# Optimization experiments

Measured on AMD Instinct MI355X. Metric: run time of the kernel, lower is better.

The kernel has to match this reference:

```python
import jax, jax.numpy as jnp
import numpy as np
from jax import lax

EXP = 3          # exp_size
TOPK = 9         # top_number
DS = 4           # down_sample (stride & kernel of conv_down)
UP = 4           # up_sample
C_CH = 64        # c
BN_EPS = 1e-5


def conv2d(x, w, b, stride, pad):
    y = lax.conv_general_dilated(x, w, (stride, stride), ((pad, pad), (pad, pad)),
                                 dimension_numbers=('NCHW', 'OIHW', 'NCHW'))
    return y + b[None, :, None, None]


def bnorm(x, g, b, m, v):
    scale = g / jnp.sqrt(v + BN_EPS)
    return (x - m[None, :, None, None]) * scale[None, :, None, None] + b[None, :, None, None]


def get_feat(x1, H, W):
    # x1: [B, C, L] flattened downsampled features
    B, C, L = x1.shape
    win = 2 * EXP + 1
    xt = jnp.transpose(x1, (0, 2, 1))                      # [B, L, C]
    # euclidean distance -> similarity 1/(1+d)
    sq = jnp.sum(xt * xt, axis=-1)                         # [B, L]
    d2 = sq[:, :, None] + sq[:, None, :] - 2.0 * jnp.einsum('blc,bmc->blm', xt, xt)
    dist = jnp.sqrt(jnp.maximum(d2, 1e-12))
    sim = 1.0 / (1.0 + dist)                               # [B, L, L]
    pad = jnp.pad(sim.reshape(B, L, H, W),
                  ((0, 0), (0, 0), (EXP, EXP), (EXP, EXP)),
                  constant_values=1e20)                    # [B, L, H+2e, W+2e]
    l = jnp.arange(L)
    row, col = l // W, l % W
    d = jnp.arange(win)
    off_i = jnp.repeat(d, win)
    off_j = jnp.tile(d, win)
    ii = row[:, None] + off_i[None, :]                     # [L, P] padded coords
    jj = col[:, None] + off_j[None, :]
    win_val = pad[:, l[:, None], ii, jj]                   # [B, L, P]
    # topk SMALLEST similarity (most dissimilar); padded 1e20 never selected
    _, idx = lax.top_k(-win_val, TOPK)                     # [B, L, k]
    h_bias = idx // win - EXP
    w_bias = idx % win - EXP
    Hf = row[None, :, None] + h_bias
    Wf = col[None, :, None] + w_bias
    index = Hf * W + Wf                                    # [B, L, k] in [0, L)
    b_idx = jnp.arange(B)[:, None, None]
    x_final = xt[b_idx, index]                             # [B, L, k, C]
    return x_final


def setup_inputs() -> dict:
    key = jax.random.key(0)
    ks = jax.random.split(key, 6)
    c = C_CH
    f32 = jnp.float32
    x = jax.random.normal(ks[0], (4, c, 256, 256), f32)
    wd = jax.random.normal(ks[1], (c, c, DS, DS), f32) * 0.05
    bd = jnp.zeros((c,), f32)
    w1 = jax.random.normal(ks[2], (c, 2 * c, 3, 3), f32) * 0.05
    b1 = jnp.zeros((c,), f32)
    wa = jax.random.normal(ks[3], (c, c, 1, 1), f32) * 0.05
    ones, zeros = jnp.ones((c,), f32), jnp.zeros((c,), f32)
    return dict(x=x,
                wd=wd, bd=bd, bnd_g=ones, bnd_b=zeros, bnd_m=zeros, bnd_v=ones,
                w1=w1, b1=b1, bn1_g=ones, bn1_b=zeros, bn1_m=zeros, bn1_v=ones,
                wa=wa, bna_g=ones, bna_b=zeros, bna_m=zeros, bna_v=ones)


def reference(x, wd, bd, bnd_g, bnd_b, bnd_m, bnd_v,
              w1, b1, bn1_g, bn1_b, bn1_m, bn1_v,
              wa, bna_g, bna_b, bna_m, bna_v):
    # conv_down: Conv(k=DS, s=DS, p=0) + BN + ReLU
    x1 = jax.nn.relu(bnorm(conv2d(x, wd, bd, DS, 0), bnd_g, bnd_b, bnd_m, bnd_v))
    B, C, H, W = x1.shape
    L = H * W
    xf = x1.reshape(B, C, L)
    x_final = get_feat(xf, H, W)                           # [B, L, k, C]
    xt = jnp.transpose(xf, (0, 2, 1))                      # [B, L, C]
    out = jnp.mean(x_final - xt[:, :, None, :], axis=2)    # [B, L, C]
    out_img = jnp.transpose(out, (0, 2, 1)).reshape(B, C, H, W)
    cat = jnp.concatenate([x1, out_img], axis=1)           # [B, 2C, H, W]
    # SENet: conv3x3 + BN + ReLU, global-avg-pool attention
    feat = jax.nn.relu(bnorm(conv2d(cat, w1, b1, 1, 1), bn1_g, bn1_b, bn1_m, bn1_v))
    att = jnp.mean(feat, axis=(2, 3), keepdims=True)       # [B, C, 1, 1]
    att = lax.conv_general_dilated(att, wa, (1, 1), ((0, 0), (0, 0)),
                                   dimension_numbers=('NCHW', 'OIHW', 'NCHW'))
    att = jax.nn.sigmoid(bnorm(att, bna_g, bna_b, bna_m, bna_v))
    out = feat * att
    # F.interpolate bilinear, align_corners=False == half-pixel resize
    return jax.image.resize(out, (B, C, H * UP, W * UP), method='bilinear')
```

## Files before the change

kernel.cpp:

```cpp
#include <hip/hip_runtime.h>
#include <hip/hip_bf16.h>
#include <stdint.h>

__device__ __forceinline__ float* catp(float* o, int p) {
    return o + (size_t)(p & 255) * 65536 + 4096 + ((p >> 8) << 12);
}
__device__ __forceinline__ double* x1hp(float* o, int q) {
    return (double*)(o + (size_t)q * 65536 + 16384);
}
__device__ __forceinline__ float wtv(const float* o, int kk, int co) {
    return o[(size_t)(kk >> 3) * 65536 + 25600 + (kk & 7) * 64 + co];
}
__device__ __forceinline__ double* wd64p(float* o, int k) {
    return (double*)(o + (size_t)(k >> 2) * 65536 + 26624) + (k & 3) * 64;
}

__global__ __launch_bounds__(256) void k0_wtrans(const float* __restrict__ w1, const float* __restrict__ wd,
                                                 float* __restrict__ o) {
    int idx = blockIdx.x * 256 + threadIdx.x;
    if (idx < 73728) {
        int co = idx & 63, kk = idx >> 6;
        o[(size_t)(kk >> 3) * 65536 + 25600 + (kk & 7) * 64 + co] = w1[co * 1152 + kk];
    } else if (idx < 139264) {
        int j = idx - 73728;
        int co = j & 63, k = j >> 6;
        wd64p(o, k)[co] = (double)wd[co * 1024 + k];
    }
}

__global__ __launch_bounds__(256) void k1_convds(
    const float* __restrict__ x, const float* __restrict__ bd,
    const float* __restrict__ g, const float* __restrict__ be,
    const float* __restrict__ m, const float* __restrict__ v,
    float* __restrict__ o)
{
    __shared__ __align__(16) double wlds[2][32 * 64];
    __shared__ __align__(16) double xlds[2][32 * 32];
    int blk = blockIdx.x;
    int jh = blk & 1, i = (blk >> 1) & 63, b = blk >> 7;
    int t = threadIdx.x;
    int tj = t & 15, tc = t >> 4;
    int s_f4j = t & 31, s_ky = (t >> 5) & 3, s_ciL = t >> 7;
    int s_kq = (s_ciL * 16 + s_ky * 4) * 32 + s_f4j;

    double acc[4][2];
    #pragma unroll
    for (int c = 0; c < 4; ++c) { acc[c][0] = 0.0; acc[c][1] = 0.0; }

    double wreg[8];
    float4 xreg;
    #pragma unroll
    for (int u = 0; u < 8; ++u) {
        int idx = t + u * 256;
        wreg[u] = wd64p(o, (idx >> 6))[idx & 63];
    }
    xreg = *(const float4*)(x + (((size_t)(b * 64 + s_ciL) * 256 + (i * 4 + s_ky)) * 256 + jh * 128 + s_f4j * 4));
    #pragma unroll
    for (int u = 0; u < 8; ++u) {
        int idx = t + u * 256;
        wlds[0][(idx >> 6) * 64 + (idx & 63)] = wreg[u];
    }
    xlds[0][s_kq]      = (double)xreg.x;
    xlds[0][s_kq + 32] = (double)xreg.y;
    xlds[0][s_kq + 64] = (double)xreg.z;
    xlds[0][s_kq + 96] = (double)xreg.w;
    __syncthreads();

    for (int p = 0; p < 32; ++p) {
        int cur = p & 1;
        if (p + 1 < 32) {
            #pragma unroll
            for (int u = 0; u < 8; ++u) {
                int idx = t + u * 256;
                wreg[u] = wd64p(o, (p + 1) * 32 + (idx >> 6))[idx & 63];
            }
            xreg = *(const float4*)(x + (((size_t)(b * 64 + (p + 1) * 2 + s_ciL) * 256 + (i * 4 + s_ky)) * 256 + jh * 128 + s_f4j * 4));
        }
        const double* wb = wlds[cur];
        const double* xb = xlds[cur];
        #pragma unroll
        for (int ciL = 0; ciL < 2; ++ciL) {
            #pragma unroll
            for (int ky = 0; ky < 4; ++ky) {
                int kq = ciL * 16 + ky * 4;
                double w_[4][4], x_[4][2];
                #pragma unroll
                for (int kx = 0; kx < 4; ++kx) {
                    const double* wp = wb + (kq + kx) * 64;
                    const double* xp = xb + (kq + kx) * 32;
                    double2 wa0 = *(const double2*)(wp + tc * 2);
                    double2 wa1 = *(const double2*)(wp + tc * 2 + 32);
                    double2 xa0 = *(const double2*)(xp + tj * 2);
                    w_[kx][0] = wa0.x; w_[kx][1] = wa0.y; w_[kx][2] = wa1.x; w_[kx][3] = wa1.y;
                    x_[kx][0] = xa0.x; x_[kx][1] = xa0.y;
                }
                #pragma unroll
                for (int c = 0; c < 4; ++c)
                    #pragma unroll
                    for (int jj = 0; jj < 2; ++jj)
                        acc[c][jj] = fma(w_[0][c], x_[0][jj],
                                     fma(w_[1][c], x_[1][jj],
                                     fma(w_[2][c], x_[2][jj],
                                     fma(w_[3][c], x_[3][jj], acc[c][jj]))));
            }
        }
        if (p + 1 < 32) {
            int nxt = (p + 1) & 1;
            #pragma unroll
            for (int u = 0; u < 8; ++u) {
                int idx = t + u * 256;
                wlds[nxt][(idx >> 6) * 64 + (idx & 63)] = wreg[u];
            }
            xlds[nxt][s_kq]      = (double)xreg.x;
            xlds[nxt][s_kq + 32] = (double)xreg.y;
            xlds[nxt][s_kq + 64] = (double)xreg.z;
            xlds[nxt][s_kq + 96] = (double)xreg.w;
            __syncthreads();
        }
    }
    #pragma unroll
    for (int c = 0; c < 4; ++c) {
        int co = ((c >> 1) << 5) + tc * 2 + (c & 1);
        double sc = (double)g[co] / sqrt((double)v[co] + 1e-5);
        double sh = (double)bd[co] - (double)m[co];
        double bb = (double)be[co];
        double o0v = fmax(0.0, (acc[c][0] + sh) * sc + bb);
        double o1v = fmax(0.0, (acc[c][1] + sh) * sc + bb);
        int pos0 = i * 64 + jh * 32 + tj * 2;
        float* cp = catp(o, b * 128 + co);
        *(float2*)(cp + pos0) = make_float2((float)o0v, (float)o1v);
        double* xh = x1hp(o, b * 64 + co);
        *(double2*)(xh + pos0) = make_double2(o0v, o1v);
    }
}

__global__ __launch_bounds__(512) void k2_feat(float* __restrict__ o)
{
    __shared__ __align__(16) char smem[29568];
    __shared__ double sqd[7 * 64];
    __shared__ int sels[64 * 9];
    double* tile_d = (double*)smem;
    double* d2s = (double*)smem;
    float* tileq = (float*)smem;
    int blk = blockIdx.x;
    int b = blk >> 6, i = blk & 63;
    int t = threadIdx.x;
    int lane = t & 63, wv = t >> 6;

    double dacc[7];
    #pragma unroll
    for (int k = 0; k < 7; ++k) dacc[k] = 0.0;
    double sq_own = 0.0;

    for (int q = 0; q < 8; ++q) {
        __syncthreads();
        for (int s = t; s < 1792; s += 512) {
            int rc = s >> 5, c2 = s & 31;
            int r = rc >> 3, c = rc & 7;
            int gr = i - 3 + r;
            if (gr >= 0 && gr <= 63) {
                const double* src = x1hp(o, b * 64 + q * 8 + c);
                *(double2*)(tile_d + rc * 66 + c2 * 2) = *(const double2*)(src + gr * 64 + c2 * 2);
            }
        }
        __syncthreads();
        if (t < 448) {
            int r = t >> 6, col = t & 63;
            int gr = i - 3 + r;
            if (gr >= 0 && gr <= 63) {
                double s = 0.0;
                #pragma unroll
                for (int c = 0; c < 8; ++c) {
                    double xv = tile_d[(r * 8 + c) * 66 + col];
                    s = fma(xv, xv, s);
                }
                sq_own += s;
            }
        }
        double xlq[8];
        #pragma unroll
        for (int c = 0; c < 8; ++c) xlq[c] = tile_d[(24 + c) * 66 + lane];
        #pragma unroll
        for (int k = 0; k < 7; ++k) {
            int oo = wv + 8 * k;
            if (oo < 49) {
                int oi = oo / 7 - 3, oj = oo % 7 - 3;
                int mi = i + oi, mj = lane + oj;
                if (mi >= 0 && mi <= 63 && mj >= 0 && mj <= 63) {
                    int r = oi + 3;
                    double dot = 0.0;
                    #pragma unroll
                    for (int c = 0; c < 8; ++c) dot = fma(xlq[c], tile_d[(r * 8 + c) * 66 + mj], dot);
                    dacc[k] += dot;
                }
            }
        }
    }
    __syncthreads();
    if (t < 448) sqd[t] = sq_own;
    __syncthreads();
    #pragma unroll
    for (int k = 0; k < 7; ++k) {
        int oo = wv + 8 * k;
        if (oo < 49) {
            int oi = oo / 7 - 3, oj = oo % 7 - 3;
            int mi = i + oi, mj = lane + oj;
            double d2 = -1e300;
            if (mi >= 0 && mi <= 63 && mj >= 0 && mj <= 63)
                d2 = sqd[192 + lane] + sqd[(oi + 3) * 64 + mj] - 2.0 * dacc[k];
            d2s[lane * 50 + oo] = d2;
        }
    }
    __syncthreads();
    if (wv == 0) {
        unsigned long long mask = 0ull;
        for (int k = 0; k < 9; ++k) {
            double best = -1e308; int bi = 0;
            for (int oo = 0; oo < 49; ++oo) {
                if ((mask >> oo) & 1ull) continue;
                double vv = d2s[lane * 50 + oo];
                if (vv > best) { best = vv; bi = oo; }
            }
            mask |= (1ull << bi);
            sels[lane * 9 + k] = bi;
        }
    }
    __syncthreads();
    int rk[9], cj[9];
    #pragma unroll
    for (int k = 0; k < 9; ++k) {
        int oo = sels[lane * 9 + k];
        rk[k] = oo / 7;
        cj[k] = lane + (oo % 7) - 3;
    }
    for (int q = 0; q < 8; ++q) {
        __syncthreads();
        for (int s = t; s < 896; s += 512) {
            int rc = s >> 4, x4 = s & 15;
            int r = rc >> 3, c = rc & 7;
            int gr = i - 3 + r;
            if (gr >= 0 && gr <= 63)
                *(float4*)(tileq + rc * 68 + x4 * 4) =
                    *(const float4*)(catp(o, b * 128 + q * 8 + c) + gr * 64 + x4 * 4);
        }
        __syncthreads();
        {
            int c = wv;
            float s = 0.f;
            #pragma unroll
            for (int k = 0; k < 9; ++k) s += tileq[(rk[k] * 8 + c) * 68 + cj[k]];
            float outv = s * (1.f / 9.f) - tileq[(24 + c) * 68 + lane];
            catp(o, b * 128 + 64 + q * 8 + c)[i * 64 + lane] = outv;
        }
    }
}

__global__ __launch_bounds__(512) void k3_conv(
    float* __restrict__ o, const float* __restrict__ b1,
    const float* __restrict__ g, const float* __restrict__ be,
    const float* __restrict__ m, const float* __restrict__ v)
{
    __shared__ __align__(16) float wlds[8 * 9 * 64];
    __shared__ __align__(16) float xlds[3 * 8 * 40];
    int blk = blockIdx.x;
    int jh = blk & 1, i = (blk >> 1) & 63, b = blk >> 7;
    int t = threadIdx.x;
    int co = t & 63, jg = t >> 6;
    float acc0 = 0.f, acc1 = 0.f, acc2 = 0.f, acc3 = 0.f;
    const float4 z4 = make_float4(0.f, 0.f, 0.f, 0.f);
    for (int st = 0; st < 16; ++st) {
        __syncthreads();
        for (int idx = t; idx < 4608; idx += 512) {
            int kk = st * 72 + (idx >> 6);
            wlds[idx] = wtv(o, kk, idx & 63);
        }
        for (int f = t; f < 240; f += 512) {
            int x4 = f % 10, rc = f / 10;
            int ry = rc >> 3, cl = rc & 7;
            int gr = i - 1 + ry;
            int col0 = jh * 32 - 4 + x4 * 4;
            float4 val = z4;
            if (gr >= 0 && gr <= 63 && col0 >= 0 && col0 <= 60)
                val = *(const float4*)(catp(o, b * 128 + st * 8 + cl) + gr * 64 + col0);
            *(float4*)(xlds + rc * 40 + x4 * 4) = val;
        }
        __syncthreads();
        for (int cl = 0; cl < 8; ++cl) {
            #pragma unroll
            for (int ry = 0; ry < 3; ++ry) {
                float w0  = wlds[(cl * 9 + ry * 3 + 0) * 64 + co];
                float w1f = wlds[(cl * 9 + ry * 3 + 1) * 64 + co];
                float w2  = wlds[(cl * 9 + ry * 3 + 2) * 64 + co];
                const float* xr = xlds + (ry * 8 + cl) * 40 + jg * 4;
                float4 q0 = *(const float4*)(xr);
                float4 q1 = *(const float4*)(xr + 4);
                float4 q2 = *(const float4*)(xr + 8);
                float xv[12] = { q0.x,q0.y,q0.z,q0.w, q1.x,q1.y,q1.z,q1.w, q2.x,q2.y,q2.z,q2.w };
                acc0 = fmaf(w0, xv[3], fmaf(w1f, xv[4], fmaf(w2, xv[5], acc0)));
                acc1 = fmaf(w0, xv[4], fmaf(w1f, xv[5], fmaf(w2, xv[6], acc1)));
                acc2 = fmaf(w0, xv[5], fmaf(w1f, xv[6], fmaf(w2, xv[7], acc2)));
                acc3 = fmaf(w0, xv[6], fmaf(w1f, xv[7], fmaf(w2, xv[8], acc3)));
            }
        }
    }
    float sc = g[co] * rsqrtf(v[co] + 1e-5f);
    float sh = b1[co] - m[co];
    float bb = be[co];
    float4 ov;
    ov.x = fmaxf(0.f, fmaf(acc0 + sh, sc, bb));
    ov.y = fmaxf(0.f, fmaf(acc1 + sh, sc, bb));
    ov.z = fmaxf(0.f, fmaf(acc2 + sh, sc, bb));
    ov.w = fmaxf(0.f, fmaf(acc3 + sh, sc, bb));
    *(float4*)(o + (size_t)(b * 64 + co) * 65536 + i * 64 + jh * 32 + jg * 4) = ov;
}

__global__ __launch_bounds__(256) void k4_mean(float* __restrict__ o) {
    int q = blockIdx.x, t = threadIdx.x;
    const float* p = o + (size_t)q * 65536;
    float s = 0.f;
    for (int k = t; k < 4096; k += 256) s += p[k];
    #pragma unroll
    for (int off = 32; off > 0; off >>= 1) s += __shfl_down(s, off, 64);
    __shared__ float red[4];
    if ((t & 63) == 0) red[t >> 6] = s;
    __syncthreads();
    if (t == 0) o[(size_t)q * 65536 + 12288] = (red[0] + red[1] + red[2] + red[3]) * (1.f / 4096.f);
}

__global__ __launch_bounds__(256) void k4_att(float* __restrict__ o, const float* __restrict__ wa,
    const float* __restrict__ g, const float* __restrict__ be, const float* __restrict__ m, const float* __restrict__ v) {
    int t = threadIdx.x;
    int b = t >> 6, co = t & 63;
    const float* wr = wa + co * 64;
    float s = 0.f;
    for (int ci = 0; ci < 64; ++ci) s = fmaf(wr[ci], o[(size_t)(b * 64 + ci) * 65536 + 12288], s);
    float sc = g[co] * rsqrtf(v[co] + 1e-5f);
    float y = fmaf(s - m[co], sc, be[co]);
    o[(size_t)t * 65536 + 12289] = 1.f / (1.f + expf(-y));
}

__global__ __launch_bounds__(1024) void k5_up(float* __restrict__ o) {
    __shared__ __align__(16) float fplane[4096];
    int bc = blockIdx.x;
    int t = threadIdx.x;
    float* slot = o + (size_t)bc * 65536;
    *(float4*)(fplane + t * 4) = *(const float4*)(slot + t * 4);
    float att = slot[12289];
    __syncthreads();
    int ox = t & 255, oyc = t >> 8;
    float fx = ox * 0.25f - 0.375f;
    int ix = (int)floorf(fx);
    float wx = fx - (float)ix;
    int x0 = ix < 0 ? 0 : ix;
    int x1 = (ix + 1 > 63) ? 63 : ix + 1;
    for (int oy = oyc * 64; oy < oyc * 64 + 64; ++oy) {
        float fy = oy * 0.25f - 0.375f;
        int iy = (int)floorf(fy);
        float wy = fy - (float)iy;
        int y0 = iy < 0 ? 0 : iy;
        int y1 = (iy + 1 > 63) ? 63 : iy + 1;
        float a  = fplane[y0 * 64 + x0], b_ = fplane[y0 * 64 + x1];
        float c_ = fplane[y1 * 64 + x0], d_ = fplane[y1 * 64 + x1];
        float top = a + wx * (b_ - a);
        float bot = c_ + wx * (d_ - c_);
        float val = (top + wy * (bot - top)) * att;
        slot[oy * 256 + ox] = val;
    }
}

extern "C" void kernel_launch(void* const* d_in, const int* in_sizes, int n_in,
                              void* d_out, int out_size, void* d_ws, size_t ws_size,
                              hipStream_t stream) {
    const float* x     = (const float*)d_in[0];
    const float* wd    = (const float*)d_in[1];
    const float* bd    = (const float*)d_in[2];
    const float* bnd_g = (const float*)d_in[3];
    const float* bnd_b = (const float*)d_in[4];
    const float* bnd_m = (const float*)d_in[5];
    const float* bnd_v = (const float*)d_in[6];
    const float* w1    = (const float*)d_in[7];
    const float* b1    = (const float*)d_in[8];
    const float* bn1_g = (const float*)d_in[9];
    const float* bn1_b = (const float*)d_in[10];
    const float* bn1_m = (const float*)d_in[11];
    const float* bn1_v = (const float*)d_in[12];
    const float* wa    = (const float*)d_in[13];
    const float* bna_g = (const float*)d_in[14];
    const float* bna_b = (const float*)d_in[15];
    const float* bna_m = (const float*)d_in[16];
    const float* bna_v = (const float*)d_in[17];

    float* o = (float*)d_out;

    hipLaunchKernelGGL(k0_wtrans, dim3(544), dim3(256), 0, stream, w1, wd, o);
    hipLaunchKernelGGL(k1_convds, dim3(512), dim3(256), 0, stream,
                       x, bd, bnd_g, bnd_b, bnd_m, bnd_v, o);
    hipLaunchKernelGGL(k2_feat, dim3(256), dim3(512), 0, stream, o);
    hipLaunchKernelGGL(k3_conv, dim3(512), dim3(512), 0, stream,
                       o, b1, bn1_g, bn1_b, bn1_m, bn1_v);
    hipLaunchKernelGGL(k4_mean, dim3(256), dim3(256), 0, stream, o);
    hipLaunchKernelGGL(k4_att, dim3(1), dim3(256), 0, stream,
                       o, wa, bna_g, bna_b, bna_m, bna_v);
    hipLaunchKernelGGL(k5_up, dim3(256), dim3(1024), 0, stream, o);
}
```

Before: 241.5 us.

## Double-buffer weight and input tiles in 3x3 conv kernel via register prefetch

The conv3x3 kernel now keeps two LDS buffers for weights and input rows. While the current channel slice is being computed, it loads the next slice into registers and stores it to the other buffer afterwards, leaving one barrier per stage instead of two. This is meant to hide global load latency behind the FMA loop. It costs double the LDS and extra registers (9 floats plus a float4), which may lower occupancy.

```diff
diff --git a/kernel.cpp b/kernel.cpp
--- a/kernel.cpp
+++ b/kernel.cpp
@@ -260,38 +260,57 @@
     const float* __restrict__ g, const float* __restrict__ be,
     const float* __restrict__ m, const float* __restrict__ v)
 {
-    __shared__ __align__(16) float wlds[8 * 9 * 64];
-    __shared__ __align__(16) float xlds[3 * 8 * 40];
+    __shared__ __align__(16) float wlds[2][8 * 9 * 64];
+    __shared__ __align__(16) float xlds[2][3 * 8 * 40];
     int blk = blockIdx.x;
     int jh = blk & 1, i = (blk >> 1) & 63, b = blk >> 7;
     int t = threadIdx.x;
     int co = t & 63, jg = t >> 6;
     float acc0 = 0.f, acc1 = 0.f, acc2 = 0.f, acc3 = 0.f;
     const float4 z4 = make_float4(0.f, 0.f, 0.f, 0.f);
+    bool xact = t < 240;
+    int x_x4 = t % 10, x_rc = t / 10;
+    int x_ry = x_rc >> 3;
+    int x_cl = x_rc & 7;
+    int x_gr = i - 1 + x_ry;
+    int x_col0 = jh * 32 - 4 + x_x4 * 4;
+    bool x_ok = xact && x_gr >= 0 && x_gr <= 63 && x_col0 >= 0 && x_col0 <= 60;
+
+    float wreg[9];
+    float4 xreg = z4;
+    #pragma unroll
+    for (int u = 0; u < 9; ++u) {
+        int idx = t + u * 512;
+        wreg[u] = wtv(o, (idx >> 6), idx & 63);
+    }
+    if (x_ok) xreg = *(const float4*)(catp(o, b * 128 + x_cl) + x_gr * 64 + x_col0);
+    #pragma unroll
+    for (int u = 0; u < 9; ++u) {
+        int idx = t + u * 512;
+        wlds[0][idx] = wreg[u];
+    }
+    if (xact) *(float4*)(&xlds[0][x_rc * 40 + x_x4 * 4]) = x_ok ? xreg : z4;
+    __syncthreads();
+
     for (int st = 0; st < 16; ++st) {
-        __syncthreads();
-        for (int idx = t; idx < 4608; idx += 512) {
-            int kk = st * 72 + (idx >> 6);
-            wlds[idx] = wtv(o, kk, idx & 63);
-        }
-        for (int f = t; f < 240; f += 512) {
-            int x4 = f % 10, rc = f / 10;
-            int ry = rc >> 3, cl = rc & 7;
-            int gr = i - 1 + ry;
-            int col0 = jh * 32 - 4 + x4 * 4;
-            float4 val = z4;
-            if (gr >= 0 && gr <= 63 && col0 >= 0 && col0 <= 60)
-                val = *(const float4*)(catp(o, b * 128 + st * 8 + cl) + gr * 64 + col0);
-            *(float4*)(xlds + rc * 40 + x4 * 4) = val;
-        }
-        __syncthreads();
+        int cur = st & 1;
+        if (st + 1 < 16) {
+            #pragma unroll
+            for (int u = 0; u < 9; ++u) {
+                int idx = t + u * 512;
+                wreg[u] = wtv(o, (st + 1) * 72 + (idx >> 6), idx & 63);
+            }
+            if (x_ok) xreg = *(const float4*)(catp(o, b * 128 + (st + 1) * 8 + x_cl) + x_gr * 64 + x_col0);
+        }
+        const float* wb = wlds[cur];
+        const float* xb = xlds[cur];
         for (int cl = 0; cl < 8; ++cl) {
             #pragma unroll
             for (int ry = 0; ry < 3; ++ry) {
-                float w0  = wlds[(cl * 9 + ry * 3 + 0) * 64 + co];
-                float w1f = wlds[(cl * 9 + ry * 3 + 1) * 64 + co];
-                float w2  = wlds[(cl * 9 + ry * 3 + 2) * 64 + co];
-                const float* xr = xlds + (ry * 8 + cl) * 40 + jg * 4;
+                float w0  = wb[(cl * 9 + ry * 3 + 0) * 64 + co];
+                float w1f = wb[(cl * 9 + ry * 3 + 1) * 64 + co];
+                float w2  = wb[(cl * 9 + ry * 3 + 2) * 64 + co];
+                const float* xr = xb + (ry * 8 + cl) * 40 + jg * 4;
                 float4 q0 = *(const float4*)(xr);
                 float4 q1 = *(const float4*)(xr + 4);
                 float4 q2 = *(const float4*)(xr + 8);
@@ -301,6 +320,16 @@
                 acc2 = fmaf(w0, xv[5], fmaf(w1f, xv[6], fmaf(w2, xv[7], acc2)));
                 acc3 = fmaf(w0, xv[6], fmaf(w1f, xv[7], fmaf(w2, xv[8], acc3)));
             }
+        }
+        if (st + 1 < 16) {
+            int nxt = (st + 1) & 1;
+            #pragma unroll
+            for (int u = 0; u < 9; ++u) {
+                int idx = t + u * 512;
+                wlds[nxt][idx] = wreg[u];
+            }
+            if (xact) *(float4*)(&xlds[nxt][x_rc * 40 + x_x4 * 4]) = x_ok ? xreg : z4;
+            __syncthreads();
         }
     }
     float sc = g[co] * rsqrtf(v[co] + 1e-5f);
```

After: 283.1 us. 17.2% more time.
